# Kernel optimization log

Measured on AMD Instinct MI355X. Metric: run time of the kernel, lower is better.

Reference implementation:

```python
import jax, jax.numpy as jnp
import numpy as np

B, S, IN_DIM, H, D = 2, 2048, 1024, 16, 64

def setup_inputs() -> dict:
    key = jax.random.key(0)
    ks = jax.random.split(key, 8)
    Q = jax.random.normal(ks[0], (B, S, IN_DIM), dtype=jnp.float32)
    K = jax.random.normal(ks[1], (B, S, IN_DIM), dtype=jnp.float32)
    V = jax.random.normal(ks[2], (B, S, IN_DIM), dtype=jnp.float32)
    # True = masked position (matches torch masked_fill_ semantics)
    attn_mask = jax.random.bernoulli(ks[3], 0.1, (B, S, S))
    scale = 1.0 / np.sqrt(IN_DIM)
    Wq = jax.random.normal(ks[4], (IN_DIM, H * D), dtype=jnp.float32) * scale
    Wk = jax.random.normal(ks[5], (IN_DIM, H * D), dtype=jnp.float32) * scale
    Wv = jax.random.normal(ks[6], (IN_DIM, H * D), dtype=jnp.float32) * scale
    Wo = jax.random.normal(ks[7], (H * D, IN_DIM), dtype=jnp.float32) * scale
    return {"Q": Q, "K": K, "V": V, "attn_mask": attn_mask,
            "Wq": Wq, "Wk": Wk, "Wv": Wv, "Wo": Wo}

def reference(Q, K, V, attn_mask, Wq, Wk, Wv, Wo):
    b, s, _ = Q.shape
    # Projections -> [B, H, S, D]
    q = (Q @ Wq).reshape(b, s, H, D).transpose(0, 2, 1, 3)
    k = (K @ Wk).reshape(b, s, H, D).transpose(0, 2, 1, 3)
    v = (V @ Wv).reshape(b, s, H, D).transpose(0, 2, 1, 3)
    scores = jnp.einsum('bhqd,bhkd->bhqk', q, k) / np.sqrt(D)
    scores = jnp.where(attn_mask[:, None, :, :], jnp.float32(-1e9), scores)
    attn = jax.nn.softmax(scores, axis=-1)
    ctx = jnp.einsum('bhqk,bhkd->bhqd', attn, v)  # [B, H, S, D]
    ctx = ctx.transpose(0, 2, 1, 3).reshape(b, s, H * D)
    return ctx @ Wo + Q
```

## Files before the change

### kernel.cpp

```cpp
#include <hip/hip_runtime.h>
#include <hip/hip_bf16.h>


#define BB   2
#define SS   2048
#define IND  1024
#define HH   16
#define DD   64

typedef __attribute__((ext_vector_type(8))) short  s8b;
typedef __attribute__((ext_vector_type(4))) short  s4b;
typedef __attribute__((ext_vector_type(4))) float  f32x4;

static __device__ __forceinline__ short f2b(float x) {
    return __builtin_bit_cast(short, __float2bfloat16(x));
}

__global__ __launch_bounds__(256) void wconv(const float* __restrict__ w0,
                                             const float* __restrict__ w1,
                                             const float* __restrict__ w2,
                                             const float* __restrict__ w3,
                                             short* __restrict__ out) {
    const int z = blockIdx.z;
    const float* src = (z == 0) ? w0 : (z == 1) ? w1 : (z == 2) ? w2 : w3;
    const float wscale = (z == 0) ? 0.125f : 1.0f;
    short* dst = out + (size_t)z * IND * IND;
    __shared__ __attribute__((aligned(16))) short ls[64][72];
    const int t  = threadIdx.x;
    const int k0 = blockIdx.y * 64;
    const int n0 = blockIdx.x * 64;
#pragma unroll
    for (int p = 0; p < 4; ++p) {
        int ch = t + p * 256;
        int r  = ch >> 4;
        int c4 = ch & 15;
        float4 v = *reinterpret_cast<const float4*>(&src[(size_t)(k0 + r) * IND + n0 + c4 * 4]);
        ls[r][c4 * 4 + 0] = f2b(v.x * wscale);
        ls[r][c4 * 4 + 1] = f2b(v.y * wscale);
        ls[r][c4 * 4 + 2] = f2b(v.z * wscale);
        ls[r][c4 * 4 + 3] = f2b(v.w * wscale);
    }
    __syncthreads();
#pragma unroll
    for (int p = 0; p < 2; ++p) {
        int ch = t + p * 256;
        int nr = ch >> 3;
        int kg = ch & 7;
        s8b o;
#pragma unroll
        for (int j = 0; j < 8; ++j) o[j] = ls[kg * 8 + j][nr];
        *reinterpret_cast<s8b*>(&dst[(size_t)(n0 + nr) * IND + k0 + kg * 8]) = o;
    }
}

__global__ __launch_bounds__(256) void maskpack(const unsigned char* __restrict__ mask,
                                                unsigned long long* __restrict__ bits) {
    __shared__ int s_flag;
    const int t = threadIdx.x;
    if (t == 0) s_flag = 0;
    __syncthreads();
    {
        int bad = 0;
#pragma unroll
        for (int i = 0; i < 16; ++i) {
            int idx = t * 16 + i;
            if ((idx & 3) && mask[idx]) bad = 1;
        }
        if (bad) s_flag = 1;
    }
    __syncthreads();
    const bool isI32 = (s_flag == 0);

    const int lane = t & 63;
    const size_t nwords = (size_t)BB * SS * SS / 64;
    size_t w = (size_t)blockIdx.x * 4 + (t >> 6);
    const size_t stride = (size_t)gridDim.x * 4;
    if (isI32) {
        const unsigned* m4 = (const unsigned*)mask;
        for (; w < nwords; w += stride) {
            unsigned long long bal = __ballot(m4[w * 64 + lane] != 0);
            if (lane == 0) bits[w] = bal;
        }
    } else {
        for (; w < nwords; w += stride) {
            unsigned long long bal = __ballot(mask[w * 64 + lane] != 0);
            if (lane == 0) bits[w] = bal;
        }
    }
}

__global__ __launch_bounds__(256) void gemm_qkv(const float* __restrict__ Aq,
                                                const float* __restrict__ Ak,
                                                const float* __restrict__ Av,
                                                const short* __restrict__ wt,
                                                short* __restrict__ qb,
                                                short* __restrict__ kb,
                                                short* __restrict__ vt) {
    __shared__ __attribute__((aligned(16))) short lsA[128 * 40];
    __shared__ __attribute__((aligned(16))) short lsB[128 * 40];
    const int z = blockIdx.z;
    const float* A  = (z == 0) ? Aq : (z == 1) ? Ak : Av;
    const short* Bt = wt + (size_t)z * IND * IND;

    const int t    = threadIdx.x;
    const int lane = t & 63;
    const int wv   = t >> 6;
    const int wr   = wv >> 1, wc = wv & 1;
    const int m0   = blockIdx.y * 128, n0 = blockIdx.x * 128;
    const int lr   = lane & 15;
    const int lg   = lane >> 4;

    f32x4 acc[4][4] = {};

    for (int k0 = 0; k0 < IND; k0 += 32) {
        __syncthreads();
#pragma unroll
        for (int p = 0; p < 4; ++p) {
            int ch = t + p * 256;
            int r = ch >> 3, c4 = ch & 7;
            float4 v = *reinterpret_cast<const float4*>(&A[(size_t)(m0 + r) * IND + k0 + c4 * 4]);
            s4b w;
            w[0] = f2b(v.x); w[1] = f2b(v.y); w[2] = f2b(v.z); w[3] = f2b(v.w);
            *reinterpret_cast<s4b*>(&lsA[r * 40 + c4 * 4]) = w;
        }
#pragma unroll
        for (int p = 0; p < 2; ++p) {
            int ch = t + p * 256;
            int r = ch >> 2, c8 = ch & 3;
            s8b v = *reinterpret_cast<const s8b*>(&Bt[(size_t)(n0 + r) * IND + k0 + c8 * 8]);
            *reinterpret_cast<s8b*>(&lsB[r * 40 + c8 * 8]) = v;
        }
        __syncthreads();

        s8b af[4], bfr[4];
#pragma unroll
        for (int mi = 0; mi < 4; ++mi)
            af[mi] = *reinterpret_cast<const s8b*>(&lsA[(wr * 64 + mi * 16 + lr) * 40 + lg * 8]);
#pragma unroll
        for (int nj = 0; nj < 4; ++nj)
            bfr[nj] = *reinterpret_cast<const s8b*>(&lsB[(wc * 64 + nj * 16 + lr) * 40 + lg * 8]);
#pragma unroll
        for (int mi = 0; mi < 4; ++mi)
#pragma unroll
            for (int nj = 0; nj < 4; ++nj)
                acc[mi][nj] = __builtin_amdgcn_mfma_f32_16x16x32_bf16(af[mi], bfr[nj], acc[mi][nj], 0, 0, 0);
    }

#pragma unroll
    for (int mi = 0; mi < 4; ++mi) {
#pragma unroll
        for (int nj = 0; nj < 4; ++nj) {
            const int mbase = m0 + wr * 64 + mi * 16 + lg * 4;
            const int n     = n0 + wc * 64 + nj * 16 + lr;
            if (z < 2) {
                short* o = z ? kb : qb;
                const int h = n >> 6, d = n & 63;
#pragma unroll
                for (int i = 0; i < 4; ++i) {
                    int m = mbase + i;
                    int b = m >> 11, s = m & 2047;
                    o[((size_t)(b * HH + h) * SS + s) * DD + d] = f2b(acc[mi][nj][i]);
                }
            } else {
                const int b = mbase >> 11, sbase = mbase & 2047;
                const int h = n >> 6, d = n & 63;
                s4b w;
#pragma unroll
                for (int i = 0; i < 4; ++i) w[i] = f2b(acc[mi][nj][i]);
                *reinterpret_cast<s4b*>(&vt[((size_t)(b * HH + h) * DD + d) * SS + sbase]) = w;
            }
        }
    }
}

__global__ __launch_bounds__(256) void attn(const short* __restrict__ qb,
                                            const short* __restrict__ kb,
                                            const short* __restrict__ vt,
                                            const unsigned* __restrict__ mbw,
                                            short* __restrict__ ctx) {
    __shared__ __attribute__((aligned(16))) short lsK[64 * 72];
    __shared__ __attribute__((aligned(16))) short lsV[64 * 72];
    __shared__ __attribute__((aligned(16))) short lsP[4][16 * 72];

    const int t    = threadIdx.x;
    const int lane = t & 63;
    const int wv   = t >> 6;
    const int bh   = blockIdx.y;
    const int b    = bh >> 4, h = bh & 15;
    const int q0   = blockIdx.x * 64 + wv * 16;
    const int lr   = lane & 15;
    const int lg   = lane >> 4;

    const unsigned sel0 = 1u << lr;
    const unsigned sel1 = sel0 << 16;
    const uint2* mrp = (const uint2*)(mbw + (size_t)(b * SS + q0 + lg * 4) * (SS / 32));

    s8b aq[2];
#pragma unroll
    for (int ks = 0; ks < 2; ++ks)
        aq[ks] = *reinterpret_cast<const s8b*>(&qb[((size_t)bh * SS + q0 + lr) * DD + ks * 32 + lg * 8]);

    s8b ones;
#pragma unroll
    for (int j = 0; j < 8; ++j) ones[j] = (short)0x3F80;

    f32x4 o[4] = {};
    float lrow[4] = {0.f, 0.f, 0.f, 0.f};

    for (int kk0 = 0; kk0 < SS; kk0 += 64) {
        __syncthreads();
#pragma unroll
        for (int p = 0; p < 2; ++p) {
            int ch = t + p * 256;
            int r = ch >> 3, c = ch & 7;
            *reinterpret_cast<s8b*>(&lsK[r * 72 + c * 8]) =
                *reinterpret_cast<const s8b*>(&kb[((size_t)bh * SS + kk0 + r) * DD + c * 8]);
            *reinterpret_cast<s8b*>(&lsV[r * 72 + c * 8]) =
                *reinterpret_cast<const s8b*>(&vt[((size_t)bh * DD + r) * SS + kk0 + c * 8]);
        }
        uint2 mw[4];
#pragma unroll
        for (int i = 0; i < 4; ++i) mw[i] = mrp[i * 32 + (kk0 >> 6)];
        __syncthreads();

        f32x4 sc[4];
#pragma unroll
        for (int nj = 0; nj < 4; ++nj) {
            s8b bk0 = *reinterpret_cast<const s8b*>(&lsK[(nj * 16 + lr) * 72 + lg * 8]);
            s8b bk1 = *reinterpret_cast<const s8b*>(&lsK[(nj * 16 + lr) * 72 + 32 + lg * 8]);
            f32x4 zz = {};
            zz     = __builtin_amdgcn_mfma_f32_16x16x32_bf16(aq[0], bk0, zz, 0, 0, 0);
            sc[nj] = __builtin_amdgcn_mfma_f32_16x16x32_bf16(aq[1], bk1, zz, 0, 0, 0);
        }

#pragma unroll
        for (int nj = 0; nj < 4; ++nj) {
            const unsigned slm = (nj & 1) ? sel1 : sel0;
#pragma unroll
            for (int i = 0; i < 4; ++i) {
                unsigned w = (nj < 2) ? mw[i].x : mw[i].y;
                float e = __expf(sc[nj][i]);
                float p = (w & slm) ? 0.f : e;
                lsP[wv][(lg * 4 + i) * 72 + nj * 16 + lr] = f2b(p);
            }
        }

        s8b pa[2];
#pragma unroll
        for (int ks = 0; ks < 2; ++ks)
            pa[ks] = *reinterpret_cast<const s8b*>(&lsP[wv][lr * 72 + ks * 32 + lg * 8]);

        f32x4 rs = {};
        rs = __builtin_amdgcn_mfma_f32_16x16x32_bf16(pa[0], ones, rs, 0, 0, 0);
        rs = __builtin_amdgcn_mfma_f32_16x16x32_bf16(pa[1], ones, rs, 0, 0, 0);

#pragma unroll
        for (int nj = 0; nj < 4; ++nj) {
            s8b bv0 = *reinterpret_cast<const s8b*>(&lsV[(nj * 16 + lr) * 72 + lg * 8]);
            s8b bv1 = *reinterpret_cast<const s8b*>(&lsV[(nj * 16 + lr) * 72 + 32 + lg * 8]);
            o[nj] = __builtin_amdgcn_mfma_f32_16x16x32_bf16(pa[0], bv0, o[nj], 0, 0, 0);
            o[nj] = __builtin_amdgcn_mfma_f32_16x16x32_bf16(pa[1], bv1, o[nj], 0, 0, 0);
        }
#pragma unroll
        for (int i = 0; i < 4; ++i) lrow[i] += rs[i];
    }

    float inv[4];
#pragma unroll
    for (int i = 0; i < 4; ++i) inv[i] = 1.0f / lrow[i];
#pragma unroll
    for (int nj = 0; nj < 4; ++nj)
#pragma unroll
        for (int i = 0; i < 4; ++i) {
            int q = q0 + lg * 4 + i;
            ctx[((size_t)(b * SS + q)) * (HH * DD) + h * DD + nj * 16 + lr] = f2b(o[nj][i] * inv[i]);
        }
}

__global__ __launch_bounds__(256) void gemm_out(const short* __restrict__ Actx,
                                                const short* __restrict__ Bt,
                                                const float* __restrict__ resid,
                                                float* __restrict__ outp) {
    __shared__ __attribute__((aligned(16))) short lsA[64 * 40];
    __shared__ __attribute__((aligned(16))) short lsB[128 * 40];
    const int t    = threadIdx.x;
    const int lane = t & 63;
    const int wv   = t >> 6;
    const int wr   = wv >> 1, wc = wv & 1;
    const int m0   = blockIdx.y * 64, n0 = blockIdx.x * 128;
    const int lr   = lane & 15;
    const int lg   = lane >> 4;

    f32x4 acc[2][4] = {};

    for (int k0 = 0; k0 < IND; k0 += 32) {
        __syncthreads();
        {
            int r = t >> 2, c8 = t & 3;
            s8b v = *reinterpret_cast<const s8b*>(&Actx[(size_t)(m0 + r) * IND + k0 + c8 * 8]);
            *reinterpret_cast<s8b*>(&lsA[r * 40 + c8 * 8]) = v;
        }
#pragma unroll
        for (int p = 0; p < 2; ++p) {
            int ch = t + p * 256;
            int r = ch >> 2, c8 = ch & 3;
            s8b v = *reinterpret_cast<const s8b*>(&Bt[(size_t)(n0 + r) * IND + k0 + c8 * 8]);
            *reinterpret_cast<s8b*>(&lsB[r * 40 + c8 * 8]) = v;
        }
        __syncthreads();

        s8b af[2], bfr[4];
#pragma unroll
        for (int mi = 0; mi < 2; ++mi)
            af[mi] = *reinterpret_cast<const s8b*>(&lsA[(wr * 32 + mi * 16 + lr) * 40 + lg * 8]);
#pragma unroll
        for (int nj = 0; nj < 4; ++nj)
            bfr[nj] = *reinterpret_cast<const s8b*>(&lsB[(wc * 64 + nj * 16 + lr) * 40 + lg * 8]);
#pragma unroll
        for (int mi = 0; mi < 2; ++mi)
#pragma unroll
            for (int nj = 0; nj < 4; ++nj)
                acc[mi][nj] = __builtin_amdgcn_mfma_f32_16x16x32_bf16(af[mi], bfr[nj], acc[mi][nj], 0, 0, 0);
    }

#pragma unroll
    for (int mi = 0; mi < 2; ++mi)
#pragma unroll
        for (int nj = 0; nj < 4; ++nj) {
            const int mbase = m0 + wr * 32 + mi * 16 + lg * 4;
            const int n     = n0 + wc * 64 + nj * 16 + lr;
#pragma unroll
            for (int i = 0; i < 4; ++i) {
                int m = mbase + i;
                outp[(size_t)m * IND + n] = acc[mi][nj][i] + resid[(size_t)m * IND + n];
            }
        }
}

extern "C" void kernel_launch(void* const* d_in, const int* in_sizes, int n_in,
                              void* d_out, int out_size, void* d_ws, size_t ws_size,
                              hipStream_t stream) {
    const float* Qin = (const float*)d_in[0];
    const float* Kin = (const float*)d_in[1];
    const float* Vin = (const float*)d_in[2];
    const unsigned char* mask = (const unsigned char*)d_in[3];
    const float* Wq = (const float*)d_in[4];
    const float* Wk = (const float*)d_in[5];
    const float* Wv = (const float*)d_in[6];
    const float* Wo = (const float*)d_in[7];

    char* ws = (char*)d_ws;
    const size_t WSZ = (size_t)IND * IND;
    short* wt  = (short*)ws;
    short* qb  = (short*)(ws + 8ull  * 1024 * 1024);
    short* kb  = (short*)(ws + 16ull * 1024 * 1024);
    short* vt  = (short*)(ws + 24ull * 1024 * 1024);
    short* ctx = (short*)(ws + 32ull * 1024 * 1024);
    unsigned long long* mbits = (unsigned long long*)(ws + 40ull * 1024 * 1024);

    wconv   <<<dim3(16, 16, 4), 256, 0, stream>>>(Wq, Wk, Wv, Wo, wt);
    maskpack<<<512, 256, 0, stream>>>(mask, mbits);
    gemm_qkv<<<dim3(8, 32, 3), 256, 0, stream>>>(Qin, Kin, Vin, wt, qb, kb, vt);
    attn    <<<dim3(SS / 64, BB * HH), 256, 0, stream>>>(qb, kb, vt, (const unsigned*)mbits, ctx);
    gemm_out<<<dim3(8, 64), 256, 0, stream>>>(ctx, wt + 3 * WSZ, Qin, (float*)d_out);
}
```

Measured before the change: 309.0 us.

## Double-buffer attention K/V via async LDS loads; pre-convert QKV inputs to bf16

```diff
diff --git a/kernel.cpp b/kernel.cpp
--- a/kernel.cpp
+++ b/kernel.cpp
@@ -7,6 +7,7 @@
 #define IND  1024
 #define HH   16
 #define DD   64
+#define MM_ELEMS 524288
 
 typedef __attribute__((ext_vector_type(8))) short  s8b;
 typedef __attribute__((ext_vector_type(4))) short  s4b;
@@ -15,6 +16,11 @@
 static __device__ __forceinline__ short f2b(float x) {
     return __builtin_bit_cast(short, __float2bfloat16(x));
 }
+
+#define GLD16(g, l)                                                             \
+    __builtin_amdgcn_global_load_lds(                                           \
+        (const __attribute__((address_space(1))) unsigned int*)(g),             \
+        (__attribute__((address_space(3))) unsigned int*)(l), 16, 0, 0)
 
 __global__ __launch_bounds__(256) void wconv(const float* __restrict__ w0,
                                              const float* __restrict__ w1,
@@ -89,9 +95,28 @@
     }
 }
 
-__global__ __launch_bounds__(256) void gemm_qkv(const float* __restrict__ Aq,
-                                                const float* __restrict__ Ak,
-                                                const float* __restrict__ Av,
+__global__ __launch_bounds__(256) void cvt3(const float* __restrict__ q,
+                                            const float* __restrict__ k,
+                                            const float* __restrict__ v,
+                                            short* __restrict__ o) {
+    const size_t nchunk = (size_t)3 * MM_ELEMS;
+    size_t i = (size_t)blockIdx.x * 256 + threadIdx.x;
+    const size_t stride = (size_t)gridDim.x * 256;
+    for (; i < nchunk; i += stride) {
+        size_t base = i * 8;
+        int z = (int)(base >> 22);
+        size_t off = base & 4194303u;
+        const float* src = (z == 0) ? q : (z == 1) ? k : v;
+        float4 a = *reinterpret_cast<const float4*>(&src[off]);
+        float4 b = *reinterpret_cast<const float4*>(&src[off + 4]);
+        s8b w;
+        w[0] = f2b(a.x); w[1] = f2b(a.y); w[2] = f2b(a.z); w[3] = f2b(a.w);
+        w[4] = f2b(b.x); w[5] = f2b(b.y); w[6] = f2b(b.z); w[7] = f2b(b.w);
+        *reinterpret_cast<s8b*>(&o[base]) = w;
+    }
+}
+
+__global__ __launch_bounds__(256) void gemm_qkv(const short* __restrict__ abf,
                                                 const short* __restrict__ wt,
                                                 short* __restrict__ qb,
                                                 short* __restrict__ kb,
@@ -99,7 +124,7 @@
     __shared__ __attribute__((aligned(16))) short lsA[128 * 40];
     __shared__ __attribute__((aligned(16))) short lsB[128 * 40];
     const int z = blockIdx.z;
-    const float* A  = (z == 0) ? Aq : (z == 1) ? Ak : Av;
+    const short* A  = abf + (size_t)z * 4194304;
     const short* Bt = wt + (size_t)z * IND * IND;
 
     const int t    = threadIdx.x;
@@ -115,13 +140,11 @@
     for (int k0 = 0; k0 < IND; k0 += 32) {
         __syncthreads();
 #pragma unroll
-        for (int p = 0; p < 4; ++p) {
+        for (int p = 0; p < 2; ++p) {
             int ch = t + p * 256;
-            int r = ch >> 3, c4 = ch & 7;
-            float4 v = *reinterpret_cast<const float4*>(&A[(size_t)(m0 + r) * IND + k0 + c4 * 4]);
-            s4b w;
-            w[0] = f2b(v.x); w[1] = f2b(v.y); w[2] = f2b(v.z); w[3] = f2b(v.w);
-            *reinterpret_cast<s4b*>(&lsA[r * 40 + c4 * 4]) = w;
+            int r = ch >> 2, c8 = ch & 3;
+            s8b v = *reinterpret_cast<const s8b*>(&A[(size_t)(m0 + r) * IND + k0 + c8 * 8]);
+            *reinterpret_cast<s8b*>(&lsA[r * 40 + c8 * 8]) = v;
         }
 #pragma unroll
         for (int p = 0; p < 2; ++p) {
@@ -178,8 +201,8 @@
                                             const short* __restrict__ vt,
                                             const unsigned* __restrict__ mbw,
                                             short* __restrict__ ctx) {
-    __shared__ __attribute__((aligned(16))) short lsK[64 * 72];
-    __shared__ __attribute__((aligned(16))) short lsV[64 * 72];
+    __shared__ __attribute__((aligned(16))) short lsK[2][64 * 64];
+    __shared__ __attribute__((aligned(16))) short lsV[2][64 * 64];
     __shared__ __attribute__((aligned(16))) short lsP[4][16 * 72];
 
     const int t    = threadIdx.x;
@@ -195,6 +218,11 @@
     const unsigned sel1 = sel0 << 16;
     const uint2* mrp = (const uint2*)(mbw + (size_t)(b * SS + q0 + lg * 4) * (SS / 32));
 
+    const int rk = lane >> 3;
+    const int ck = (lane & 7) ^ rk;
+    const short* kbase = kb + (size_t)bh * SS * DD;
+    const short* vbase = vt + (size_t)bh * DD * SS;
+
     s8b aq[2];
 #pragma unroll
     for (int ks = 0; ks < 2; ++ks)
@@ -207,27 +235,42 @@
     f32x4 o[4] = {};
     float lrow[4] = {0.f, 0.f, 0.f, 0.f};
 
+#pragma unroll
+    for (int c = 0; c < 2; ++c) {
+        int chunk = wv + c * 4;
+        int row = chunk * 8 + rk;
+        GLD16(&kbase[(size_t)row * DD + ck * 8], &lsK[0][chunk * 512]);
+        GLD16(&vbase[(size_t)row * SS + ck * 8], &lsV[0][chunk * 512]);
+    }
+
+    int cur = 0;
     for (int kk0 = 0; kk0 < SS; kk0 += 64) {
+        uint2 mw[4];
+#pragma unroll
+        for (int i = 0; i < 4; ++i) mw[i] = mrp[i * 32 + (kk0 >> 6)];
+
         __syncthreads();
-#pragma unroll
-        for (int p = 0; p < 2; ++p) {
-            int ch = t + p * 256;
-            int r = ch >> 3, c = ch & 7;
-            *reinterpret_cast<s8b*>(&lsK[r * 72 + c * 8]) =
-                *reinterpret_cast<const s8b*>(&kb[((size_t)bh * SS + kk0 + r) * DD + c * 8]);
-            *reinterpret_cast<s8b*>(&lsV[r * 72 + c * 8]) =
-                *reinterpret_cast<const s8b*>(&vt[((size_t)bh * DD + r) * SS + kk0 + c * 8]);
-        }
-        uint2 mw[4];
-#pragma unroll
-        for (int i = 0; i < 4; ++i) mw[i] = mrp[i * 32 + (kk0 >> 6)];
-        __syncthreads();
+
+        if (kk0 + 64 < SS) {
+#pragma unroll
+            for (int c = 0; c < 2; ++c) {
+                int chunk = wv + c * 4;
+                int row = chunk * 8 + rk;
+                GLD16(&kbase[(size_t)(kk0 + 64 + row) * DD + ck * 8], &lsK[cur ^ 1][chunk * 512]);
+                GLD16(&vbase[(size_t)row * SS + kk0 + 64 + ck * 8], &lsV[cur ^ 1][chunk * 512]);
+            }
+        }
+
+        const short* Kc = lsK[cur];
+        const short* Vc = lsV[cur];
 
         f32x4 sc[4];
 #pragma unroll
         for (int nj = 0; nj < 4; ++nj) {
-            s8b bk0 = *reinterpret_cast<const s8b*>(&lsK[(nj * 16 + lr) * 72 + lg * 8]);
-            s8b bk1 = *reinterpret_cast<const s8b*>(&lsK[(nj * 16 + lr) * 72 + 32 + lg * 8]);
+            const int R  = nj * 16 + lr;
+            const int sw = R & 7;
+            s8b bk0 = *reinterpret_cast<const s8b*>(&Kc[R * 64 + ((lg ^ sw) << 3)]);
+            s8b bk1 = *reinterpret_cast<const s8b*>(&Kc[R * 64 + (((lg ^ 4) ^ sw) << 3)]);
             f32x4 zz = {};
             zz     = __builtin_amdgcn_mfma_f32_16x16x32_bf16(aq[0], bk0, zz, 0, 0, 0);
             sc[nj] = __builtin_amdgcn_mfma_f32_16x16x32_bf16(aq[1], bk1, zz, 0, 0, 0);
@@ -256,13 +299,17 @@
 
 #pragma unroll
         for (int nj = 0; nj < 4; ++nj) {
-            s8b bv0 = *reinterpret_cast<const s8b*>(&lsV[(nj * 16 + lr) * 72 + lg * 8]);
-            s8b bv1 = *reinterpret_cast<const s8b*>(&lsV[(nj * 16 + lr) * 72 + 32 + lg * 8]);
+            const int R  = nj * 16 + lr;
+            const int sw = R & 7;
+            s8b bv0 = *reinterpret_cast<const s8b*>(&Vc[R * 64 + ((lg ^ sw) << 3)]);
+            s8b bv1 = *reinterpret_cast<const s8b*>(&Vc[R * 64 + (((lg ^ 4) ^ sw) << 3)]);
             o[nj] = __builtin_amdgcn_mfma_f32_16x16x32_bf16(pa[0], bv0, o[nj], 0, 0, 0);
             o[nj] = __builtin_amdgcn_mfma_f32_16x16x32_bf16(pa[1], bv1, o[nj], 0, 0, 0);
         }
 #pragma unroll
         for (int i = 0; i < 4; ++i) lrow[i] += rs[i];
+
+        cur ^= 1;
     }
 
     float inv[4];
@@ -355,12 +402,14 @@
     short* qb  = (short*)(ws + 8ull  * 1024 * 1024);
     short* kb  = (short*)(ws + 16ull * 1024 * 1024);
     short* vt  = (short*)(ws + 24ull * 1024 * 1024);
-    short* ctx = (short*)(ws + 32ull * 1024 * 1024);
-    unsigned long long* mbits = (unsigned long long*)(ws + 40ull * 1024 * 1024);
+    unsigned long long* mbits = (unsigned long long*)(ws + 32ull * 1024 * 1024);
+    short* abf = (short*)(ws + 36ull * 1024 * 1024);
+    short* ctx = (short*)(ws + 36ull * 1024 * 1024);
 
     wconv   <<<dim3(16, 16, 4), 256, 0, stream>>>(Wq, Wk, Wv, Wo, wt);
     maskpack<<<512, 256, 0, stream>>>(mask, mbits);
-    gemm_qkv<<<dim3(8, 32, 3), 256, 0, stream>>>(Qin, Kin, Vin, wt, qb, kb, vt);
+    cvt3    <<<2048, 256, 0, stream>>>(Qin, Kin, Vin, abf);
+    gemm_qkv<<<dim3(8, 32, 3), 256, 0, stream>>>(abf, wt, qb, kb, vt);
     attn    <<<dim3(SS / 64, BB * HH), 256, 0, stream>>>(qb, kb, vt, (const unsigned*)mbits, ctx);
     gemm_out<<<dim3(8, 64), 256, 0, stream>>>(ctx, wt + 3 * WSZ, Qin, (float*)d_out);
 }
```

Result: slower. 328.9 us (+6.5%).
